# Kernel tuning notes

Measured on AMD Instinct MI355X. Metric: run time of the kernel, lower is better.

## Reference

```python
import jax, jax.numpy as jnp
import numpy as np

DIM = 256
NUM_HEAD = 8
HEAD_DIM = DIM // NUM_HEAD
SCALE = HEAD_DIM ** -0.5


def setup_inputs() -> dict:
    key = jax.random.key(0)
    ks = jax.random.split(key, 8)
    B, NQ, NK = 8, 512, 4096
    state = jax.random.normal(ks[0], (B, NQ, DIM), dtype=jnp.float32)
    pointcloud = jax.random.normal(ks[1], (B, NK, DIM), dtype=jnp.float32)
    s = 0.02
    Wq = jax.random.normal(ks[2], (DIM, DIM), dtype=jnp.float32) * s
    bq = jnp.zeros((DIM,), dtype=jnp.float32)
    Wkv = jax.random.normal(ks[3], (DIM, 2 * DIM), dtype=jnp.float32) * s
    bkv = jnp.zeros((2 * DIM,), dtype=jnp.float32)
    Wo = jax.random.normal(ks[4], (DIM, DIM), dtype=jnp.float32) * s
    bo = jnp.zeros((DIM,), dtype=jnp.float32)
    return {"state": state, "pointcloud": pointcloud, "Wq": Wq, "bq": bq,
            "Wkv": Wkv, "bkv": bkv, "Wo": Wo, "bo": bo}


def reference(state, pointcloud, Wq, bq, Wkv, bkv, Wo, bo):
    # q: [b, nq, dim]; kv: [b, nk, 2*dim]
    q = state @ Wq + bq
    kv = pointcloud @ Wkv + bkv
    k, v = jnp.split(kv, 2, axis=-1)

    def split_heads(x):
        b, n, _ = x.shape
        return x.reshape(b, n, NUM_HEAD, HEAD_DIM).transpose(0, 2, 1, 3)  # b h n d

    q, k, v = split_heads(q), split_heads(k), split_heads(v)
    attn = jnp.einsum('bhqd,bhkd->bhqk', q, k) * SCALE
    attn = jax.nn.softmax(attn, axis=-1)
    out = jnp.einsum('bhqk,bhkd->bhqd', attn, v)
    b, h, nq, d = out.shape
    out = out.transpose(0, 2, 1, 3).reshape(b, nq, h * d)
    return out @ Wo + bo
```

## Files before the change

### kernel.cpp

```cpp
#include <hip/hip_runtime.h>

typedef unsigned short u16;
typedef unsigned int   u32;
typedef __bf16 bf16x8 __attribute__((ext_vector_type(8)));
typedef float  f32x4  __attribute__((ext_vector_type(4)));
typedef float  f32x16 __attribute__((ext_vector_type(16)));
typedef u32    u32x4  __attribute__((ext_vector_type(4)));
typedef u16    u16x8  __attribute__((ext_vector_type(8)));

#define DEVINL __device__ __forceinline__

DEVINL void glds16(const void* g, void* l) {
  __builtin_amdgcn_global_load_lds((const __attribute__((address_space(1))) u32*)g,
                                   (__attribute__((address_space(3))) u32*)l, 16, 0, 0);
}

DEVINL u16 f2bf(float f) {
  u32 u = __builtin_bit_cast(u32, f);
  u32 r = u + 0x7fffu + ((u >> 16) & 1u);
  return (u16)(r >> 16);
}

__global__ __launch_bounds__(256) void castw_k(const float* __restrict__ Wq,
                                               const float* __restrict__ Wkv,
                                               const float* __restrict__ Wo,
                                               u16* __restrict__ WqT, u16* __restrict__ WkvT,
                                               u16* __restrict__ WoT) {
  int i = blockIdx.x * 256 + threadIdx.x;
  if (i < 65536) {
    int n = i >> 8, k = i & 255;
    WqT[i] = f2bf(Wq[k * 256 + n]);
  } else if (i < 196608) {
    int j = i - 65536; int n = j >> 8, k = j & 255;
    WkvT[j] = f2bf(Wkv[k * 512 + n]);
  } else {
    int j = i - 196608; int n = j >> 8, k = j & 255;
    WoT[j] = f2bf(Wo[k * 256 + n]);
  }
}

template<int EPI, bool A_F32>
__global__ __launch_bounds__(256) void gemm_k(const void* __restrict__ Ap,
                                              const u16* __restrict__ Bt,
                                              const float* __restrict__ bias,
                                              void* __restrict__ Cp, void* __restrict__ C2p,
                                              int M, int N, int nmt, float scale) {
  const int K = 256;
  __shared__ __align__(16) u16 As[128 * 64];
  __shared__ __align__(16) u16 Bs[128 * 64];
  int tid = threadIdx.x, lane = tid & 63, w = tid >> 6;
  int g = lane >> 4, ln15 = lane & 15;
  int bid = blockIdx.x;
  int mt = bid % nmt, nt = bid / nmt;
  int arow0 = mt * 128, bcol0 = nt * 128;
  int wr = w >> 1, wc = w & 1;
  f32x4 acc[4][4] = {};

  for (int kt = 0; kt < 4; ++kt) {
    if (kt) __syncthreads();
    if (A_F32) {
      const float* A = (const float*)Ap;
      #pragma unroll
      for (int i = 0; i < 4; ++i) {
        int c = i * 256 + tid; int row = c >> 3, k8 = c & 7;
        const float* src = A + (arow0 + row) * K + kt * 64 + k8 * 8;
        f32x4 f0 = *(const f32x4*)src, f1 = *(const f32x4*)(src + 4);
        u16x8 hh;
        hh[0]=f2bf(f0[0]); hh[1]=f2bf(f0[1]); hh[2]=f2bf(f0[2]); hh[3]=f2bf(f0[3]);
        hh[4]=f2bf(f1[0]); hh[5]=f2bf(f1[1]); hh[6]=f2bf(f1[2]); hh[7]=f2bf(f1[3]);
        int idx = row * 8 + (k8 ^ (row & 7));
        *(u16x8*)&As[idx * 8] = hh;
      }
    } else {
      const u16* A = (const u16*)Ap;
      #pragma unroll
      for (int i = 0; i < 4; ++i) {
        int c = i * 256 + tid; int row = c >> 3, seg = c & 7;
        const u16* src = A + (arow0 + row) * K + kt * 64 + (seg ^ (row & 7)) * 8;
        glds16(src, (char*)As + (i * 256 + w * 64) * 16);
      }
    }
    #pragma unroll
    for (int i = 0; i < 4; ++i) {
      int c = i * 256 + tid; int row = c >> 3, seg = c & 7;
      const u16* src = Bt + (bcol0 + row) * K + kt * 64 + (seg ^ (row & 7)) * 8;
      glds16(src, (char*)Bs + (i * 256 + w * 64) * 16);
    }
    __syncthreads();
    #pragma unroll
    for (int kk = 0; kk < 2; ++kk) {
      bf16x8 af[4], bfr[4];
      #pragma unroll
      for (int mi = 0; mi < 4; ++mi) {
        int row = wr * 64 + mi * 16 + ln15;
        int idx = row * 8 + ((kk * 4 + g) ^ (row & 7));
        af[mi] = __builtin_bit_cast(bf16x8, *(const u32x4*)&As[idx * 8]);
      }
      #pragma unroll
      for (int ni = 0; ni < 4; ++ni) {
        int row = wc * 64 + ni * 16 + ln15;
        int idx = row * 8 + ((kk * 4 + g) ^ (row & 7));
        bfr[ni] = __builtin_bit_cast(bf16x8, *(const u32x4*)&Bs[idx * 8]);
      }
      #pragma unroll
      for (int mi = 0; mi < 4; ++mi)
        #pragma unroll
        for (int ni = 0; ni < 4; ++ni)
          acc[mi][ni] = __builtin_amdgcn_mfma_f32_16x16x32_bf16(af[mi], bfr[ni], acc[mi][ni], 0, 0, 0);
    }
  }
  #pragma unroll
  for (int mi = 0; mi < 4; ++mi) {
    #pragma unroll
    for (int ni = 0; ni < 4; ++ni) {
      int col = bcol0 + wc * 64 + ni * 16 + ln15;
      float bv = bias[col];
      #pragma unroll
      for (int r = 0; r < 4; ++r) {
        int row = arow0 + wr * 64 + mi * 16 + g * 4 + r;
        float v = acc[mi][ni][r] + bv;
        if (EPI == 0) {
          ((float*)Cp)[row * N + col] = v;
        } else if (EPI == 1) {
          ((u16*)Cp)[row * N + col] = f2bf(v * scale);
        } else {
          int b = row >> 12, nk = row & 4095;
          if (col < 256) {
            int h = col >> 5, d = col & 31;
            ((u16*)Cp)[(((b << 3) + h) * 4096 + nk) * 32 + d] = f2bf(v);
          } else {
            int c2 = col - 256; int h = c2 >> 5, d = c2 & 31;
            ((u16*)C2p)[(((b << 3) + h) * 4096 + nk) * 32 + d] = f2bf(v);
          }
        }
      }
    }
  }
}

__global__ __launch_bounds__(256) void attn_k(const u16* __restrict__ qb,
                                              const u16* __restrict__ kb,
                                              const u16* __restrict__ vb,
                                              u16* __restrict__ ob) {
  __shared__ __align__(16) u16 Ks[2][4 * 64 * 8];
  __shared__ __align__(16) u16 Vt[2][32 * 64];
  int tid = threadIdx.x, lane = tid & 63, w = tid >> 6;
  int hi = lane >> 5, ln31 = lane & 31;
  int bid = blockIdx.x;
  int bh = bid & 63, qblk = bid >> 6;
  int b = bh >> 3, h = bh & 7;
  const u16* khead = kb + bh * (4096 * 32);
  const u16* vhead = vb + bh * (4096 * 32);
  int qrow0 = b * 512 + qblk * 128 + w * 32;

  bf16x8 qf[2];
  #pragma unroll
  for (int ks = 0; ks < 2; ++ks) {
    const u16* src = qb + (qrow0 + ln31) * 256 + h * 32 + ks * 16 + hi * 8;
    qf[ks] = __builtin_bit_cast(bf16x8, *(const u32x4*)src);
  }

  f32x16 O = {};
  float den = 0.f;
  int vrow = tid >> 2, vdc = tid & 3;

  auto loadV = [&](int kt) -> u32x4 {
    return *(const u32x4*)(vhead + (kt * 64 + vrow) * 32 + vdc * 8);
  };
  auto stage = [&](int buf, int kt, u32x4 vv) {
    glds16(khead + (kt * 64 + lane) * 32 + w * 8, (char*)&Ks[buf][0] + w * 64 * 16);
    u16x8 us = __builtin_bit_cast(u16x8, vv);
    #pragma unroll
    for (int j = 0; j < 8; ++j) {
      int d = vdc * 8 + j;
      int cs = (vrow >> 3) ^ j ^ (vdc << 1);
      Vt[buf][d * 64 + cs * 8 + (vrow & 7)] = us[j];
    }
  };

  u32x4 vv = loadV(0);
  stage(0, 0, vv);
  vv = loadV(1);
  __syncthreads();

  for (int kt = 0; kt < 64; ++kt) {
    int buf = kt & 1;
    if (kt + 1 < 64) {
      stage(buf ^ 1, kt + 1, vv);
      vv = loadV(kt + 2 < 64 ? kt + 2 : 63);
    }
    f32x16 sT[2] = {};
    #pragma unroll
    for (int ks = 0; ks < 2; ++ks) {
      #pragma unroll
      for (int mt = 0; mt < 2; ++mt) {
        const u16* ka = &Ks[buf][((ks * 2 + hi) * 64 + mt * 32 + ln31) * 8];
        bf16x8 kf = __builtin_bit_cast(bf16x8, *(const u32x4*)ka);
        sT[mt] = __builtin_amdgcn_mfma_f32_32x32x16_bf16(kf, qf[ks], sT[mt], 0, 0, 0);
      }
    }
    u32 pa[4][4];
    #pragma unroll
    for (int mt = 0; mt < 2; ++mt) {
      float p[16];
      #pragma unroll
      for (int r = 0; r < 16; ++r) {
        p[r] = __builtin_amdgcn_exp2f(sT[mt][r]);
      }
      #pragma unroll
      for (int r = 0; r < 16; ++r) den += p[r];
      u32 pk0[4], pk1[4];
      #pragma unroll
      for (int c = 0; c < 4; ++c) {
        asm("v_cvt_pk_bf16_f32 %0, %1, %2" : "=v"(pk0[c]) : "v"(p[4*c+0]), "v"(p[4*c+1]));
        asm("v_cvt_pk_bf16_f32 %0, %1, %2" : "=v"(pk1[c]) : "v"(p[4*c+2]), "v"(p[4*c+3]));
      }
      u32 a0 = pk0[0], b0 = pk0[1];
      asm("v_permlane32_swap_b32 %0, %1" : "+v"(a0), "+v"(b0));
      u32 a1 = pk1[0], b1 = pk1[1];
      asm("v_permlane32_swap_b32 %0, %1" : "+v"(a1), "+v"(b1));
      u32 a2 = pk0[2], b2 = pk0[3];
      asm("v_permlane32_swap_b32 %0, %1" : "+v"(a2), "+v"(b2));
      u32 a3 = pk1[2], b3 = pk1[3];
      asm("v_permlane32_swap_b32 %0, %1" : "+v"(a3), "+v"(b3));
      pa[mt*2+0][0] = a0; pa[mt*2+0][1] = a1; pa[mt*2+0][2] = b0; pa[mt*2+0][3] = b1;
      pa[mt*2+1][0] = a2; pa[mt*2+1][1] = a3; pa[mt*2+1][2] = b2; pa[mt*2+1][3] = b3;
    }
    #pragma unroll
    for (int kst = 0; kst < 4; ++kst) {
      int cs = (kst * 2 + hi) ^ (ln31 & 7) ^ ((ln31 >> 3) << 1);
      const u16* va = &Vt[buf][ln31 * 64 + cs * 8];
      bf16x8 vf = __builtin_bit_cast(bf16x8, *(const u32x4*)va);
      u32x4 paw = {pa[kst][0], pa[kst][1], pa[kst][2], pa[kst][3]};
      O = __builtin_amdgcn_mfma_f32_32x32x16_bf16(__builtin_bit_cast(bf16x8, paw), vf, O, 0, 0, 0);
    }
    __syncthreads();
  }

  den += __shfl_xor(den, 32);
  #pragma unroll
  for (int r = 0; r < 16; ++r) {
    int qr = 8 * (r >> 2) + 4 * hi + (r & 3);
    float dq = __shfl(den, qr);
    float ov = O[r] / dq;
    ob[(qrow0 + qr) * 256 + h * 32 + ln31] = f2bf(ov);
  }
}

extern "C" void kernel_launch(void* const* d_in, const int* in_sizes, int n_in,
                              void* d_out, int out_size, void* d_ws, size_t ws_size,
                              hipStream_t stream) {
  const float* state = (const float*)d_in[0];
  const float* pc    = (const float*)d_in[1];
  const float* Wq    = (const float*)d_in[2];
  const float* bq    = (const float*)d_in[3];
  const float* Wkv   = (const float*)d_in[4];
  const float* bkv   = (const float*)d_in[5];
  const float* Wo    = (const float*)d_in[6];
  const float* bo    = (const float*)d_in[7];
  char* ws = (char*)d_ws;
  u16* WqT  = (u16*)(ws);
  u16* WkvT = (u16*)(ws + 131072);
  u16* WoT  = (u16*)(ws + 393216);
  u16* qb   = (u16*)(ws + 524288);
  u16* kb   = (u16*)(ws + 2621440);
  u16* vb   = (u16*)(ws + 19398656);
  u16* ob   = (u16*)(ws + 36175872);

  castw_k<<<1024, 256, 0, stream>>>(Wq, Wkv, Wo, WqT, WkvT, WoT);
  const float QSCL = 0.17677669529663687f * 1.4426950408889634f;
  gemm_k<1, true ><<<64,   256, 0, stream>>>(state, WqT, bq, qb, nullptr, 4096, 256, 32, QSCL);
  gemm_k<2, true ><<<1024, 256, 0, stream>>>(pc, WkvT, bkv, kb, vb, 32768, 512, 256, 1.f);
  attn_k<<<256, 256, 0, stream>>>(qb, kb, vb, ob);
  gemm_k<0, false><<<64,   256, 0, stream>>>(ob, WoT, bo, d_out, nullptr, 4096, 256, 32, 1.f);
}
```

Before: 187.2 us.

## Split attention keys across four wave groups and swizzle KV GEMM blocks by XCD

The attention kernel now runs 1024 threads per block, where four groups of waves each process a quarter of the 4096 keys for the same 128 queries. Partial outputs and denominators are then reduced through shared memory before the final normalisation. This quadruples the waves available to hide latency, given that the grid has only 256 blocks. Separately, the KV projection GEMM remaps block IDs so consecutive tiles sharing an A row land on the same XCD for better L2 reuse. The cost is a larger shared-memory footprint, block-wide syncs with more waves, and an extra reduction step.

Measured after the change: 151.0 us. 1.24x faster.

```diff
diff --git a/kernel.cpp b/kernel.cpp
--- a/kernel.cpp
+++ b/kernel.cpp
@@ -39,7 +39,7 @@
   }
 }
 
-template<int EPI, bool A_F32>
+template<int EPI, bool A_F32, bool XCDSWZ>
 __global__ __launch_bounds__(256) void gemm_k(const void* __restrict__ Ap,
                                               const u16* __restrict__ Bt,
                                               const float* __restrict__ bias,
@@ -51,7 +51,13 @@
   int tid = threadIdx.x, lane = tid & 63, w = tid >> 6;
   int g = lane >> 4, ln15 = lane & 15;
   int bid = blockIdx.x;
-  int mt = bid % nmt, nt = bid / nmt;
+  int mt, nt;
+  if (XCDSWZ) {
+    int u = (bid & 7) * (gridDim.x >> 3) + (bid >> 3);
+    mt = u >> 2; nt = u & 3;
+  } else {
+    mt = bid % nmt; nt = bid / nmt;
+  }
   int arow0 = mt * 128, bcol0 = nt * 128;
   int wr = w >> 1, wc = w & 1;
   f32x4 acc[4][4] = {};
@@ -138,20 +144,25 @@
   }
 }
 
-__global__ __launch_bounds__(256) void attn_k(const u16* __restrict__ qb,
-                                              const u16* __restrict__ kb,
-                                              const u16* __restrict__ vb,
-                                              u16* __restrict__ ob) {
-  __shared__ __align__(16) u16 Ks[2][4 * 64 * 8];
-  __shared__ __align__(16) u16 Vt[2][32 * 64];
+__global__ __launch_bounds__(1024, 4) void attn_k(const u16* __restrict__ qb,
+                                                  const u16* __restrict__ kb,
+                                                  const u16* __restrict__ vb,
+                                                  u16* __restrict__ ob) {
+  __shared__ __align__(16) char smem[65536];
   int tid = threadIdx.x, lane = tid & 63, w = tid >> 6;
   int hi = lane >> 5, ln31 = lane & 31;
+  int q = w & 3, s = w >> 2;
+  int stid = tid & 255;
+  int ws2 = (stid >> 6);
   int bid = blockIdx.x;
   int bh = bid & 63, qblk = bid >> 6;
   int b = bh >> 3, h = bh & 7;
   const u16* khead = kb + bh * (4096 * 32);
   const u16* vhead = vb + bh * (4096 * 32);
-  int qrow0 = b * 512 + qblk * 128 + w * 32;
+  int qrow0 = b * 512 + qblk * 128 + q * 32;
+
+  u16* Ks = (u16*)smem;
+  u16* Vt = (u16*)(smem + 32768);
 
   bf16x8 qf[2];
   #pragma unroll
@@ -162,19 +173,21 @@
 
   f32x16 O = {};
   float den = 0.f;
-  int vrow = tid >> 2, vdc = tid & 3;
-
-  auto loadV = [&](int kt) -> u32x4 {
-    return *(const u32x4*)(vhead + (kt * 64 + vrow) * 32 + vdc * 8);
+  int vrow = stid >> 2, vdc = stid & 3;
+
+  auto loadV = [&](int t) -> u32x4 {
+    return *(const u32x4*)(vhead + (((s * 16 + t) * 64) + vrow) * 32 + vdc * 8);
   };
-  auto stage = [&](int buf, int kt, u32x4 vv) {
-    glds16(khead + (kt * 64 + lane) * 32 + w * 8, (char*)&Ks[buf][0] + w * 64 * 16);
+  auto stage = [&](int buf, int t, u32x4 vv) {
+    u16* ksb = Ks + (s * 2 + buf) * 2048;
+    u16* vtb = Vt + (s * 2 + buf) * 2048;
+    glds16(khead + (((s * 16 + t) * 64) + lane) * 32 + ws2 * 8, (char*)ksb + ws2 * 64 * 16);
     u16x8 us = __builtin_bit_cast(u16x8, vv);
     #pragma unroll
     for (int j = 0; j < 8; ++j) {
       int d = vdc * 8 + j;
       int cs = (vrow >> 3) ^ j ^ (vdc << 1);
-      Vt[buf][d * 64 + cs * 8 + (vrow & 7)] = us[j];
+      vtb[d * 64 + cs * 8 + (vrow & 7)] = us[j];
     }
   };
 
@@ -183,18 +196,20 @@
   vv = loadV(1);
   __syncthreads();
 
-  for (int kt = 0; kt < 64; ++kt) {
-    int buf = kt & 1;
-    if (kt + 1 < 64) {
-      stage(buf ^ 1, kt + 1, vv);
-      vv = loadV(kt + 2 < 64 ? kt + 2 : 63);
-    }
+  for (int t = 0; t < 16; ++t) {
+    int buf = t & 1;
+    if (t + 1 < 16) {
+      stage(buf ^ 1, t + 1, vv);
+      vv = loadV(t + 2 < 16 ? t + 2 : 15);
+    }
+    const u16* ksb = Ks + (s * 2 + buf) * 2048;
+    const u16* vtb = Vt + (s * 2 + buf) * 2048;
     f32x16 sT[2] = {};
     #pragma unroll
     for (int ks = 0; ks < 2; ++ks) {
       #pragma unroll
       for (int mt = 0; mt < 2; ++mt) {
-        const u16* ka = &Ks[buf][((ks * 2 + hi) * 64 + mt * 32 + ln31) * 8];
+        const u16* ka = &ksb[((ks * 2 + hi) * 64 + mt * 32 + ln31) * 8];
         bf16x8 kf = __builtin_bit_cast(bf16x8, *(const u32x4*)ka);
         sT[mt] = __builtin_amdgcn_mfma_f32_32x32x16_bf16(kf, qf[ks], sT[mt], 0, 0, 0);
       }
@@ -204,9 +219,7 @@
     for (int mt = 0; mt < 2; ++mt) {
       float p[16];
       #pragma unroll
-      for (int r = 0; r < 16; ++r) {
-        p[r] = __builtin_amdgcn_exp2f(sT[mt][r]);
-      }
+      for (int r = 0; r < 16; ++r) p[r] = __builtin_amdgcn_exp2f(sT[mt][r]);
       #pragma unroll
       for (int r = 0; r < 16; ++r) den += p[r];
       u32 pk0[4], pk1[4];
@@ -229,7 +242,7 @@
     #pragma unroll
     for (int kst = 0; kst < 4; ++kst) {
       int cs = (kst * 2 + hi) ^ (ln31 & 7) ^ ((ln31 >> 3) << 1);
-      const u16* va = &Vt[buf][ln31 * 64 + cs * 8];
+      const u16* va = &vtb[ln31 * 64 + cs * 8];
       bf16x8 vf = __builtin_bit_cast(bf16x8, *(const u32x4*)va);
       u32x4 paw = {pa[kst][0], pa[kst][1], pa[kst][2], pa[kst][3]};
       O = __builtin_amdgcn_mfma_f32_32x32x16_bf16(__builtin_bit_cast(bf16x8, paw), vf, O, 0, 0, 0);
@@ -237,13 +250,31 @@
     __syncthreads();
   }
 
-  den += __shfl_xor(den, 32);
-  #pragma unroll
-  for (int r = 0; r < 16; ++r) {
-    int qr = 8 * (r >> 2) + 4 * hi + (r & 3);
-    float dq = __shfl(den, qr);
-    float ov = O[r] / dq;
-    ob[(qrow0 + qr) * 256 + h * 32 + ln31] = f2bf(ov);
+  float* po = (float*)smem;
+  float* pd = (float*)(smem + 49152);
+  if (s != 0) {
+    int base = ((q * 3 + (s - 1)) * 64 + lane) * 16;
+    #pragma unroll
+    for (int r = 0; r < 16; ++r) po[base + r] = O[r];
+    pd[(q * 3 + (s - 1)) * 64 + lane] = den;
+  }
+  __syncthreads();
+  if (s == 0) {
+    #pragma unroll
+    for (int j = 0; j < 3; ++j) {
+      int base = ((q * 3 + j) * 64 + lane) * 16;
+      #pragma unroll
+      for (int r = 0; r < 16; ++r) O[r] += po[base + r];
+      den += pd[(q * 3 + j) * 64 + lane];
+    }
+    den += __shfl_xor(den, 32);
+    #pragma unroll
+    for (int r = 0; r < 16; ++r) {
+      int qr = 8 * (r >> 2) + 4 * hi + (r & 3);
+      float dq = __shfl(den, qr);
+      float ov = O[r] / dq;
+      ob[(qrow0 + qr) * 256 + h * 32 + ln31] = f2bf(ov);
+    }
   }
 }
 
@@ -269,8 +300,8 @@
 
   castw_k<<<1024, 256, 0, stream>>>(Wq, Wkv, Wo, WqT, WkvT, WoT);
   const float QSCL = 0.17677669529663687f * 1.4426950408889634f;
-  gemm_k<1, true ><<<64,   256, 0, stream>>>(state, WqT, bq, qb, nullptr, 4096, 256, 32, QSCL);
-  gemm_k<2, true ><<<1024, 256, 0, stream>>>(pc, WkvT, bkv, kb, vb, 32768, 512, 256, 1.f);
-  attn_k<<<256, 256, 0, stream>>>(qb, kb, vb, ob);
-  gemm_k<0, false><<<64,   256, 0, stream>>>(ob, WoT, bo, d_out, nullptr, 4096, 256, 32, 1.f);
-}
+  gemm_k<1, true,  false><<<64,   256, 0, stream>>>(state, WqT, bq, qb, nullptr, 4096, 256, 32, QSCL);
+  gemm_k<2, true,  true ><<<1024, 256, 0, stream>>>(pc, WkvT, bkv, kb, vb, 32768, 512, 256, 1.f);
+  attn_k<<<256, 1024, 0, stream>>>(qb, kb, vb, ob);
+  gemm_k<0, false, false><<<64,   256, 0, stream>>>(ob, WoT, bo, d_out, nullptr, 4096, 256, 32, 1.f);
+}
```

## Split attention over key range, merge partials in output GEMM, fuse Q/KV GEMMs

Applied to the files above, without the earlier changes.

Attention now splits the 4096 keys into four 1024-key slices, so it launches 1024 blocks instead of 256 and fills more of the GPU. Each slice writes unnormalised fp32 partial outputs and row sums. The output projection GEMM adds the four partials, divides by the summed denominators, and converts to bf16 while loading A. The Q and KV projection GEMMs are merged into a single launch, and the KV part gets an XCD-aware block swizzle. The price is extra fp32 partial traffic of about 16 MB written and read back. The split merge is only exact because the softmax uses no max subtraction.

After: 171.3 us. -8.5%, faster.

```diff
diff --git a/kernel.cpp b/kernel.cpp
--- a/kernel.cpp
+++ b/kernel.cpp
@@ -39,31 +39,33 @@
   }
 }
 
-template<int EPI, bool A_F32>
-__global__ __launch_bounds__(256) void gemm_k(const void* __restrict__ Ap,
-                                              const u16* __restrict__ Bt,
-                                              const float* __restrict__ bias,
-                                              void* __restrict__ Cp, void* __restrict__ C2p,
-                                              int M, int N, int nmt, float scale) {
+template<int EPI, int ASRC, bool XCDSWZ>
+DEVINL void gemm_body(const void* __restrict__ Ap, const u16* __restrict__ Bt,
+                      const float* __restrict__ bias, void* __restrict__ Cp,
+                      void* __restrict__ C2p, const float* __restrict__ Dp,
+                      u16* As, u16* Bs, int N, int nmt, float scale, int bid, int nblk) {
   const int K = 256;
-  __shared__ __align__(16) u16 As[128 * 64];
-  __shared__ __align__(16) u16 Bs[128 * 64];
   int tid = threadIdx.x, lane = tid & 63, w = tid >> 6;
   int g = lane >> 4, ln15 = lane & 15;
-  int bid = blockIdx.x;
-  int mt = bid % nmt, nt = bid / nmt;
+  int mt, nt;
+  if (XCDSWZ) {
+    int u = (bid & 7) * (nblk >> 3) + (bid >> 3);
+    mt = u >> 2; nt = u & 3;
+  } else {
+    mt = bid % nmt; nt = bid / nmt;
+  }
   int arow0 = mt * 128, bcol0 = nt * 128;
   int wr = w >> 1, wc = w & 1;
   f32x4 acc[4][4] = {};
 
   for (int kt = 0; kt < 4; ++kt) {
     if (kt) __syncthreads();
-    if (A_F32) {
+    if (ASRC == 1) {
       const float* A = (const float*)Ap;
       #pragma unroll
       for (int i = 0; i < 4; ++i) {
         int c = i * 256 + tid; int row = c >> 3, k8 = c & 7;
-        const float* src = A + (arow0 + row) * K + kt * 64 + k8 * 8;
+        const float* src = A + (size_t)(arow0 + row) * K + kt * 64 + k8 * 8;
         f32x4 f0 = *(const f32x4*)src, f1 = *(const f32x4*)(src + 4);
         u16x8 hh;
         hh[0]=f2bf(f0[0]); hh[1]=f2bf(f0[1]); hh[2]=f2bf(f0[2]); hh[3]=f2bf(f0[3]);
@@ -71,19 +73,43 @@
         int idx = row * 8 + (k8 ^ (row & 7));
         *(u16x8*)&As[idx * 8] = hh;
       }
+    } else if (ASRC == 2) {
+      const float* A = (const float*)Ap;
+      #pragma unroll
+      for (int i = 0; i < 4; ++i) {
+        int c = i * 256 + tid; int row = c >> 3, k8 = c & 7;
+        int col0 = kt * 64 + k8 * 8;
+        int h = col0 >> 5;
+        size_t base = (size_t)(arow0 + row) * 256 + col0;
+        f32x4 lo = {}, hi4 = {};
+        float dsum = 0.f;
+        #pragma unroll
+        for (int ss = 0; ss < 4; ++ss) {
+          const float* p = A + ss * 1048576;
+          lo  += *(const f32x4*)(p + base);
+          hi4 += *(const f32x4*)(p + base + 4);
+          dsum += Dp[(ss * 4096 + arow0 + row) * 8 + h];
+        }
+        float inv = 1.0f / dsum;
+        u16x8 hh;
+        hh[0]=f2bf(lo[0]*inv);  hh[1]=f2bf(lo[1]*inv);  hh[2]=f2bf(lo[2]*inv);  hh[3]=f2bf(lo[3]*inv);
+        hh[4]=f2bf(hi4[0]*inv); hh[5]=f2bf(hi4[1]*inv); hh[6]=f2bf(hi4[2]*inv); hh[7]=f2bf(hi4[3]*inv);
+        int idx = row * 8 + (k8 ^ (row & 7));
+        *(u16x8*)&As[idx * 8] = hh;
+      }
     } else {
       const u16* A = (const u16*)Ap;
       #pragma unroll
       for (int i = 0; i < 4; ++i) {
         int c = i * 256 + tid; int row = c >> 3, seg = c & 7;
-        const u16* src = A + (arow0 + row) * K + kt * 64 + (seg ^ (row & 7)) * 8;
+        const u16* src = A + (size_t)(arow0 + row) * K + kt * 64 + (seg ^ (row & 7)) * 8;
         glds16(src, (char*)As + (i * 256 + w * 64) * 16);
       }
     }
     #pragma unroll
     for (int i = 0; i < 4; ++i) {
       int c = i * 256 + tid; int row = c >> 3, seg = c & 7;
-      const u16* src = Bt + (bcol0 + row) * K + kt * 64 + (seg ^ (row & 7)) * 8;
+      const u16* src = Bt + (size_t)(bcol0 + row) * K + kt * 64 + (seg ^ (row & 7)) * 8;
       glds16(src, (char*)Bs + (i * 256 + w * 64) * 16);
     }
     __syncthreads();
@@ -120,43 +146,72 @@
         int row = arow0 + wr * 64 + mi * 16 + g * 4 + r;
         float v = acc[mi][ni][r] + bv;
         if (EPI == 0) {
-          ((float*)Cp)[row * N + col] = v;
+          ((float*)Cp)[(size_t)row * N + col] = v;
         } else if (EPI == 1) {
-          ((u16*)Cp)[row * N + col] = f2bf(v * scale);
+          ((u16*)Cp)[(size_t)row * N + col] = f2bf(v * scale);
         } else {
           int b = row >> 12, nk = row & 4095;
           if (col < 256) {
             int h = col >> 5, d = col & 31;
-            ((u16*)Cp)[(((b << 3) + h) * 4096 + nk) * 32 + d] = f2bf(v);
+            ((u16*)Cp)[((size_t)((b << 3) + h) * 4096 + nk) * 32 + d] = f2bf(v);
           } else {
             int c2 = col - 256; int h = c2 >> 5, d = c2 & 31;
-            ((u16*)C2p)[(((b << 3) + h) * 4096 + nk) * 32 + d] = f2bf(v);
+            ((u16*)C2p)[((size_t)((b << 3) + h) * 4096 + nk) * 32 + d] = f2bf(v);
           }
         }
       }
     }
   }
+}
+
+__global__ __launch_bounds__(256) void gemm12_k(const float* __restrict__ state,
+                                                const float* __restrict__ pc,
+                                                const u16* __restrict__ WqT,
+                                                const u16* __restrict__ WkvT,
+                                                const float* __restrict__ bq,
+                                                const float* __restrict__ bkv,
+                                                u16* __restrict__ qbuf, u16* __restrict__ kbuf,
+                                                u16* __restrict__ vbuf, float qscl) {
+  __shared__ __align__(16) u16 As[128 * 64];
+  __shared__ __align__(16) u16 Bs[128 * 64];
+  int bid = blockIdx.x;
+  if (bid < 1024) {
+    gemm_body<2, 1, true >(pc, WkvT, bkv, kbuf, vbuf, nullptr, As, Bs, 512, 256, 1.f, bid, 1024);
+  } else {
+    gemm_body<1, 1, false>(state, WqT, bq, qbuf, nullptr, nullptr, As, Bs, 256, 32, qscl, bid - 1024, 64);
+  }
+}
+
+__global__ __launch_bounds__(256) void gemm3_k(const float* __restrict__ Op,
+                                               const u16* __restrict__ WoT,
+                                               const float* __restrict__ bo,
+                                               float* __restrict__ out,
+                                               const float* __restrict__ Dp) {
+  __shared__ __align__(16) u16 As[128 * 64];
+  __shared__ __align__(16) u16 Bs[128 * 64];
+  gemm_body<0, 2, false>(Op, WoT, bo, out, nullptr, Dp, As, Bs, 256, 32, 1.f, blockIdx.x, 64);
 }
 
 __global__ __launch_bounds__(256) void attn_k(const u16* __restrict__ qb,
                                               const u16* __restrict__ kb,
                                               const u16* __restrict__ vb,
-                                              u16* __restrict__ ob) {
-  __shared__ __align__(16) u16 Ks[2][4 * 64 * 8];
-  __shared__ __align__(16) u16 Vt[2][32 * 64];
+                                              float* __restrict__ Op,
+                                              float* __restrict__ Dp) {
+  __shared__ __align__(16) u16 Ks[2][2048];
+  __shared__ __align__(16) u16 Vt[2][2048];
   int tid = threadIdx.x, lane = tid & 63, w = tid >> 6;
   int hi = lane >> 5, ln31 = lane & 31;
   int bid = blockIdx.x;
-  int bh = bid & 63, qblk = bid >> 6;
+  int qblk = bid >> 8, r2 = bid & 255, bh = r2 >> 2, s = r2 & 3;
   int b = bh >> 3, h = bh & 7;
-  const u16* khead = kb + bh * (4096 * 32);
-  const u16* vhead = vb + bh * (4096 * 32);
+  const u16* khead = kb + ((size_t)bh * 4096 + s * 1024) * 32;
+  const u16* vhead = vb + ((size_t)bh * 4096 + s * 1024) * 32;
   int qrow0 = b * 512 + qblk * 128 + w * 32;
 
   bf16x8 qf[2];
   #pragma unroll
   for (int ks = 0; ks < 2; ++ks) {
-    const u16* src = qb + (qrow0 + ln31) * 256 + h * 32 + ks * 16 + hi * 8;
+    const u16* src = qb + (size_t)(qrow0 + ln31) * 256 + h * 32 + ks * 16 + hi * 8;
     qf[ks] = __builtin_bit_cast(bf16x8, *(const u32x4*)src);
   }
 
@@ -164,11 +219,11 @@
   float den = 0.f;
   int vrow = tid >> 2, vdc = tid & 3;
 
-  auto loadV = [&](int kt) -> u32x4 {
-    return *(const u32x4*)(vhead + (kt * 64 + vrow) * 32 + vdc * 8);
+  auto loadV = [&](int t) -> u32x4 {
+    return *(const u32x4*)(vhead + ((size_t)t * 64 + vrow) * 32 + vdc * 8);
   };
-  auto stage = [&](int buf, int kt, u32x4 vv) {
-    glds16(khead + (kt * 64 + lane) * 32 + w * 8, (char*)&Ks[buf][0] + w * 64 * 16);
+  auto stage = [&](int buf, int t, u32x4 vv) {
+    glds16(khead + ((size_t)t * 64 + lane) * 32 + w * 8, (char*)&Ks[buf][0] + w * 1024);
     u16x8 us = __builtin_bit_cast(u16x8, vv);
     #pragma unroll
     for (int j = 0; j < 8; ++j) {
@@ -183,11 +238,11 @@
   vv = loadV(1);
   __syncthreads();
 
-  for (int kt = 0; kt < 64; ++kt) {
-    int buf = kt & 1;
-    if (kt + 1 < 64) {
-      stage(buf ^ 1, kt + 1, vv);
-      vv = loadV(kt + 2 < 64 ? kt + 2 : 63);
+  for (int t = 0; t < 16; ++t) {
+    int buf = t & 1;
+    if (t + 1 < 16) {
+      stage(buf ^ 1, t + 1, vv);
+      vv = loadV(t + 2 < 16 ? t + 2 : 15);
     }
     f32x16 sT[2] = {};
     #pragma unroll
@@ -204,9 +259,7 @@
     for (int mt = 0; mt < 2; ++mt) {
       float p[16];
       #pragma unroll
-      for (int r = 0; r < 16; ++r) {
-        p[r] = __builtin_amdgcn_exp2f(sT[mt][r]);
-      }
+      for (int r = 0; r < 16; ++r) p[r] = __builtin_amdgcn_exp2f(sT[mt][r]);
       #pragma unroll
       for (int r = 0; r < 16; ++r) den += p[r];
       u32 pk0[4], pk1[4];
@@ -238,13 +291,13 @@
   }
 
   den += __shfl_xor(den, 32);
+  float* op = Op + (size_t)s * 1048576;
   #pragma unroll
   for (int r = 0; r < 16; ++r) {
     int qr = 8 * (r >> 2) + 4 * hi + (r & 3);
-    float dq = __shfl(den, qr);
-    float ov = O[r] / dq;
-    ob[(qrow0 + qr) * 256 + h * 32 + ln31] = f2bf(ov);
-  }
+    op[(size_t)(qrow0 + qr) * 256 + h * 32 + ln31] = O[r];
+  }
+  if (lane < 32) Dp[(size_t)(s * 4096 + qrow0 + ln31) * 8 + h] = den;
 }
 
 extern "C" void kernel_launch(void* const* d_in, const int* in_sizes, int n_in,
@@ -259,18 +312,18 @@
   const float* Wo    = (const float*)d_in[6];
   const float* bo    = (const float*)d_in[7];
   char* ws = (char*)d_ws;
-  u16* WqT  = (u16*)(ws);
-  u16* WkvT = (u16*)(ws + 131072);
-  u16* WoT  = (u16*)(ws + 393216);
-  u16* qb   = (u16*)(ws + 524288);
-  u16* kb   = (u16*)(ws + 2621440);
-  u16* vb   = (u16*)(ws + 19398656);
-  u16* ob   = (u16*)(ws + 36175872);
+  u16*   WqT  = (u16*)(ws);
+  u16*   WkvT = (u16*)(ws + 131072);
+  u16*   WoT  = (u16*)(ws + 393216);
+  u16*   qb   = (u16*)(ws + 524288);
+  u16*   kb   = (u16*)(ws + 2621440);
+  u16*   vb   = (u16*)(ws + 19398656);
+  float* Op   = (float*)(ws + 36175872);
+  float* Dp   = (float*)(ws + 52953088);
 
   castw_k<<<1024, 256, 0, stream>>>(Wq, Wkv, Wo, WqT, WkvT, WoT);
   const float QSCL = 0.17677669529663687f * 1.4426950408889634f;
-  gemm_k<1, true ><<<64,   256, 0, stream>>>(state, WqT, bq, qb, nullptr, 4096, 256, 32, QSCL);
-  gemm_k<2, true ><<<1024, 256, 0, stream>>>(pc, WkvT, bkv, kb, vb, 32768, 512, 256, 1.f);
-  attn_k<<<256, 256, 0, stream>>>(qb, kb, vb, ob);
-  gemm_k<0, false><<<64,   256, 0, stream>>>(ob, WoT, bo, d_out, nullptr, 4096, 256, 32, 1.f);
-}
+  gemm12_k<<<1088, 256, 0, stream>>>(state, pc, WqT, WkvT, bq, bkv, qb, kb, vb, QSCL);
+  attn_k<<<1024, 256, 0, stream>>>(qb, kb, vb, Op, Dp);
+  gemm3_k<<<64, 256, 0, stream>>>(Op, WoT, bo, (float*)d_out, Dp);
+}
```
